# Optimization experiments

Measured on AMD Instinct MI355X. Metric: run time of the kernel, lower is better.

## Reference

```python
import jax, jax.numpy as jnp
import numpy as np

NUM_ENTS = 20000
NUM_RELS = 500
DIM = 256
BATCH = 32
GAMMA = 12.0
EPSILON = 2.0
EMB_RANGE = (GAMMA + EPSILON) / DIM  # embedding_range
PI = 3.1415926235897933


def setup_inputs() -> dict:
    key = jax.random.key(0)
    k1, k2, k3, k4 = jax.random.split(key, 4)
    # xavier_normal for 2-D params: std = sqrt(2/(fan_in+fan_out))
    std_e = float(np.sqrt(2.0 / (NUM_ENTS + 2 * DIM)))
    std_r = float(np.sqrt(2.0 / (NUM_RELS + 3 * DIM)))
    emb_e = jax.random.normal(k1, (NUM_ENTS, 2 * DIM), dtype=jnp.float32) * std_e
    emb_rel = jax.random.normal(k2, (NUM_RELS, 3 * DIM), dtype=jnp.float32) * std_r
    e1 = jax.random.randint(k3, (BATCH,), 0, NUM_ENTS, dtype=jnp.int32)
    rel = jax.random.randint(k4, (BATCH,), 0, NUM_RELS, dtype=jnp.int32)
    e2_multi = jax.random.uniform(jax.random.fold_in(key, 7), (BATCH, NUM_ENTS), dtype=jnp.float32)
    phase_weight = jnp.full((1, 1), 0.5 * EMB_RANGE, dtype=jnp.float32)
    modulus_weight = jnp.full((1, 1), 1.0, dtype=jnp.float32)
    return {
        "g": 0,
        "e1": e1,
        "rel": rel,
        "e2_multi": e2_multi,
        "emb_e": emb_e,
        "emb_rel": emb_rel,
        "phase_weight": phase_weight,
        "modulus_weight": modulus_weight,
    }


def reference(g, e1, rel, e2_multi, emb_e, emb_rel, phase_weight, modulus_weight):
    head = emb_e[e1]            # (B, 2D)
    r = emb_rel[rel]            # (B, 3D)
    tail = emb_e                # (N, 2D)

    phase_head, mod_head = jnp.split(head, 2, axis=-1)            # (B, D) each
    phase_rel, mod_rel, bias_rel = jnp.split(r, 3, axis=-1)       # (B, D) each
    phase_tail, mod_tail = jnp.split(tail, 2, axis=-1)            # (N, D) each

    scale = EMB_RANGE / PI
    phase_head = phase_head / scale
    phase_rel = phase_rel / scale
    phase_tail = phase_tail / scale

    # (B, N, D) broadcast
    phase_score = (phase_head + phase_rel)[:, None, :] - phase_tail[None, :, :]

    mod_rel = jnp.abs(mod_rel)
    bias_rel = jnp.minimum(bias_rel, 1.0)
    bias_rel = jnp.where(bias_rel < -mod_rel, -mod_rel, bias_rel)

    r_score = (mod_head * (mod_rel + bias_rel))[:, None, :] \
        - mod_tail[None, :, :] * (1.0 - bias_rel)[:, None, :]      # (B, N, D)

    phase_term = jnp.sum(jnp.abs(jnp.sin(phase_score / 2.0)), axis=-1) * phase_weight  # (B, N)
    r_term = jnp.linalg.norm(r_score, axis=-1) * modulus_weight                          # (B, N)

    return jax.nn.sigmoid(GAMMA - (phase_term + r_term))
```

## Files before the change

### kernel.cpp

```cpp
#include <hip/hip_runtime.h>
#include <math.h>


#define D_   256
#define N_   20000
#define NT   16
#define NBLK (N_ / NT)
#define AP   264

#define K2S 4.571428571428571f

typedef short short8 __attribute__((ext_vector_type(8)));
typedef float f32x4  __attribute__((ext_vector_type(4)));

__device__ __forceinline__ float sinrev_(float x) { return __builtin_amdgcn_sinf(x); }

__device__ __forceinline__ short bf16r(float x) {
    union { float f; unsigned u; } v; v.f = x;
    unsigned r = (v.u + 0x7FFFu + ((v.u >> 16) & 1u)) >> 16;
    return (short)r;
}

__device__ __forceinline__ short8 pack8(float4 a, float4 b, bool sq) {
    float v[8] = {a.x, a.y, a.z, a.w, b.x, b.y, b.z, b.w};
    short8 r;
#pragma unroll
    for (int i = 0; i < 8; ++i) { float x = sq ? v[i] * v[i] : v[i]; r[i] = bf16r(x); }
    return r;
}

__global__ __launch_bounds__(512, 6)
void hake_fused(const int* __restrict__ e1, const int* __restrict__ rel,
                const float* __restrict__ emb_e, const float* __restrict__ emb_rel,
                const float* __restrict__ pw_p, const float* __restrict__ mw_p,
                float* __restrict__ out)
{
    __shared__ short A1[32 * AP];
    __shared__ short A2[32 * AP];
    __shared__ float U[4352];
    __shared__ float S0p[16][32];
    __shared__ float S0[32];

    const int t  = threadIdx.x;
    const int l  = t & 63;
    const int w  = t >> 6;
    const int b  = t & 31;
    const int g  = t >> 5;
    const int d0 = g * 16;
    const int fr = l & 15;
    const int hi = l >> 4;
    const int n0 = blockIdx.x * NT;

    const int term  = w >> 2;
    const int dbase = (w & 3) * 64;
    const float* mtp = emb_e + (size_t)(n0 + fr) * (2 * D_) + D_;
    float4 bva0 = *(const float4*)(mtp + dbase + hi * 8);
    float4 bvb0 = *(const float4*)(mtp + dbase + hi * 8 + 4);
    float4 bva1 = *(const float4*)(mtp + dbase + 32 + hi * 8);
    float4 bvb1 = *(const float4*)(mtp + dbase + 32 + hi * 8 + 4);

    const float* prow0 = emb_e + (size_t)(n0 + w * 2) * (2 * D_);
    const float* prow1 = emb_e + (size_t)(n0 + w * 2 + 1) * (2 * D_);
    float4 pv0 = *(const float4*)(prow0 + l * 4);
    float4 pv1 = *(const float4*)(prow1 + l * 4);

    float ar[16];
    {
        const int he = e1[b], hr = rel[b];
        const float* be = emb_e  + (size_t)he * (2 * D_);
        const float* br = emb_rel + (size_t)hr * (3 * D_);
        float a1v[16], a2v[16];
        float s0 = 0.0f;
#pragma unroll
        for (int q = 0; q < 4; ++q) {
            float4 ph4 = *(const float4*)(be + d0 + q * 4);
            float4 pq4 = *(const float4*)(br + d0 + q * 4);
            float4 mh4 = *(const float4*)(be + D_ + d0 + q * 4);
            float4 mr4 = *(const float4*)(br + D_ + d0 + q * 4);
            float4 bi4 = *(const float4*)(br + 2 * D_ + d0 + q * 4);
            float phv[4] = {ph4.x, ph4.y, ph4.z, ph4.w};
            float pqv[4] = {pq4.x, pq4.y, pq4.z, pq4.w};
            float mhv[4] = {mh4.x, mh4.y, mh4.z, mh4.w};
            float mrv[4] = {mr4.x, mr4.y, mr4.z, mr4.w};
            float biv[4] = {bi4.x, bi4.y, bi4.z, bi4.w};
#pragma unroll
            for (int k = 0; k < 4; ++k) {
                const int i = q * 4 + k;
                ar[i] = (phv[k] + pqv[k]) * K2S;
                float mr = fabsf(mrv[k]);
                float bi = fminf(biv[k], 1.0f);
                bi = (bi < -mr) ? -mr : bi;
                float cc = 1.0f - bi;
                float mh = mhv[k] * (mr + bi);
                a1v[i] = cc * cc;
                a2v[i] = -2.0f * mh * cc;
                s0 = fmaf(mh, mh, s0);
            }
        }
        short8 w1a, w1b, w2a, w2b;
#pragma unroll
        for (int i = 0; i < 8; ++i) {
            w1a[i] = bf16r(a1v[i]);     w1b[i] = bf16r(a1v[8 + i]);
            w2a[i] = bf16r(a2v[i]);     w2b[i] = bf16r(a2v[8 + i]);
        }
        *(short8*)(&A1[b * AP + d0])     = w1a;
        *(short8*)(&A1[b * AP + d0 + 8]) = w1b;
        *(short8*)(&A2[b * AP + d0])     = w2a;
        *(short8*)(&A2[b * AP + d0 + 8]) = w2b;
        S0p[g][b] = s0;
    }
    __syncthreads();

    if (t < 32) {
        float s = 0.0f;
#pragma unroll
        for (int q = 0; q < 16; ++q) s += S0p[q][t];
        S0[t] = s;
    }

    {
        short8 bf0 = pack8(bva0, bvb0, term == 0);
        short8 bf1 = pack8(bva1, bvb1, term == 0);
        const short* At = term ? A2 : A1;
        short8 a00 = *(const short8*)(At + fr * AP + dbase + hi * 8);
        short8 a01 = *(const short8*)(At + fr * AP + dbase + 32 + hi * 8);
        short8 a10 = *(const short8*)(At + (16 + fr) * AP + dbase + hi * 8);
        short8 a11 = *(const short8*)(At + (16 + fr) * AP + dbase + 32 + hi * 8);
        f32x4 acc0 = {0.f, 0.f, 0.f, 0.f};
        f32x4 acc1 = {0.f, 0.f, 0.f, 0.f};
        acc0 = __builtin_amdgcn_mfma_f32_16x16x32_bf16(a00, bf0, acc0, 0, 0, 0);
        acc0 = __builtin_amdgcn_mfma_f32_16x16x32_bf16(a01, bf1, acc0, 0, 0, 0);
        acc1 = __builtin_amdgcn_mfma_f32_16x16x32_bf16(a10, bf0, acc1, 0, 0, 0);
        acc1 = __builtin_amdgcn_mfma_f32_16x16x32_bf16(a11, bf1, acc1, 0, 0, 0);
#pragma unroll
        for (int r = 0; r < 4; ++r) {
            U[(w * 32 + hi * 4 + r) * 17 + fr]      = acc0[r];
            U[(w * 32 + 16 + hi * 4 + r) * 17 + fr] = acc1[r];
        }
    }
    __syncthreads();

    const int fn = t >> 5, fb = t & 31;
    float rr = 0.0f;
#pragma unroll
    for (int ww = 0; ww < 8; ++ww) rr += U[(ww * 32 + fb) * 17 + fn];
    __syncthreads();

    float4* Pp = (float4*)U;
    Pp[(w * 2) * 64 + l]     = make_float4(pv0.x * K2S, pv0.y * K2S, pv0.z * K2S, pv0.w * K2S);
    Pp[(w * 2 + 1) * 64 + l] = make_float4(pv1.x * K2S, pv1.y * K2S, pv1.z * K2S, pv1.w * K2S);
    __syncthreads();

    float sph[NT];
#pragma unroll
    for (int j = 0; j < NT; ++j) sph[j] = 0.0f;
#pragma unroll
    for (int q = 0; q < 4; ++q) {
#pragma unroll
        for (int j = 0; j < NT; ++j) {
            float4 tv = Pp[j * 64 + g * 4 + q];
            sph[j] += fabsf(sinrev_(ar[q * 4 + 0] - tv.x));
            sph[j] += fabsf(sinrev_(ar[q * 4 + 1] - tv.y));
            sph[j] += fabsf(sinrev_(ar[q * 4 + 2] - tv.z));
            sph[j] += fabsf(sinrev_(ar[q * 4 + 3] - tv.w));
        }
    }

#pragma unroll
    for (int j = 0; j < NT; ++j) sph[j] += __shfl_xor(sph[j], 32, 64);
    __syncthreads();
    if (l < 32) {
#pragma unroll
        for (int j = 0; j < NT; ++j) U[(w * 16 + j) * 32 + l] = sph[j];
    }
    __syncthreads();

    {
        float pa = 0.0f;
#pragma unroll
        for (int ww = 0; ww < 8; ++ww) pa += U[(ww * 16 + fn) * 32 + fb];
        float rfull = fmaxf(rr + S0[fb], 0.0f);
        float z = fmaf(pa, pw_p[0], sqrtf(rfull) * mw_p[0]) - 12.0f;
        out[(size_t)fb * N_ + (n0 + fn)] = 1.0f / (1.0f + __expf(z));
    }
}

extern "C" void kernel_launch(void* const* d_in, const int* in_sizes, int n_in,
                              void* d_out, int out_size, void* d_ws, size_t ws_size,
                              hipStream_t stream)
{
    const int*   e1      = (const int*)d_in[1];
    const int*   rel     = (const int*)d_in[2];
    const float* emb_e   = (const float*)d_in[4];
    const float* emb_rel = (const float*)d_in[5];
    const float* pw      = (const float*)d_in[6];
    const float* mw      = (const float*)d_in[7];
    float* out = (float*)d_out;

    hipLaunchKernelGGL(hake_fused, dim3(NBLK), dim3(512), 0, stream,
                       e1, rel, emb_e, emb_rel, pw, mw, out);
}
```

Before: 41.76 us.

## Replace per-pair sine with angle-difference identity using precomputed sin/cos

```diff
diff --git a/kernel.cpp b/kernel.cpp
--- a/kernel.cpp
+++ b/kernel.cpp
@@ -14,6 +14,7 @@
 typedef float f32x4  __attribute__((ext_vector_type(4)));
 
 __device__ __forceinline__ float sinrev_(float x) { return __builtin_amdgcn_sinf(x); }
+__device__ __forceinline__ float cosrev_(float x) { return __builtin_amdgcn_cosf(x); }
 
 __device__ __forceinline__ short bf16r(float x) {
     union { float f; unsigned u; } v; v.f = x;
@@ -35,11 +36,13 @@
                 const float* __restrict__ pw_p, const float* __restrict__ mw_p,
                 float* __restrict__ out)
 {
-    __shared__ short A1[32 * AP];
-    __shared__ short A2[32 * AP];
+    __shared__ __align__(16) char ABP[2 * 32 * AP * 2];
     __shared__ float U[4352];
     __shared__ float S0p[16][32];
     __shared__ float S0[32];
+
+    short* A1 = (short*)ABP;
+    short* A2 = (short*)(ABP + 32 * AP * 2);
 
     const int t  = threadIdx.x;
     const int l  = t & 63;
@@ -61,32 +64,29 @@
 
     const float* prow0 = emb_e + (size_t)(n0 + w * 2) * (2 * D_);
     const float* prow1 = emb_e + (size_t)(n0 + w * 2 + 1) * (2 * D_);
-    float4 pv0 = *(const float4*)(prow0 + l * 4);
-    float4 pv1 = *(const float4*)(prow1 + l * 4);
-
-    float ar[16];
-    {
-        const int he = e1[b], hr = rel[b];
-        const float* be = emb_e  + (size_t)he * (2 * D_);
-        const float* br = emb_rel + (size_t)hr * (3 * D_);
+    float2 lp00 = *(const float2*)(prow0 + 2 * l);
+    float2 lp01 = *(const float2*)(prow0 + 128 + 2 * l);
+    float2 lp10 = *(const float2*)(prow1 + 2 * l);
+    float2 lp11 = *(const float2*)(prow1 + 128 + 2 * l);
+
+    const int he = e1[b], hr = rel[b];
+    const float* be = emb_e  + (size_t)he * (2 * D_);
+    const float* br = emb_rel + (size_t)hr * (3 * D_);
+
+    {
         float a1v[16], a2v[16];
         float s0 = 0.0f;
 #pragma unroll
         for (int q = 0; q < 4; ++q) {
-            float4 ph4 = *(const float4*)(be + d0 + q * 4);
-            float4 pq4 = *(const float4*)(br + d0 + q * 4);
             float4 mh4 = *(const float4*)(be + D_ + d0 + q * 4);
             float4 mr4 = *(const float4*)(br + D_ + d0 + q * 4);
             float4 bi4 = *(const float4*)(br + 2 * D_ + d0 + q * 4);
-            float phv[4] = {ph4.x, ph4.y, ph4.z, ph4.w};
-            float pqv[4] = {pq4.x, pq4.y, pq4.z, pq4.w};
             float mhv[4] = {mh4.x, mh4.y, mh4.z, mh4.w};
             float mrv[4] = {mr4.x, mr4.y, mr4.z, mr4.w};
             float biv[4] = {bi4.x, bi4.y, bi4.z, bi4.w};
 #pragma unroll
             for (int k = 0; k < 4; ++k) {
                 const int i = q * 4 + k;
-                ar[i] = (phv[k] + pqv[k]) * K2S;
                 float mr = fabsf(mrv[k]);
                 float bi = fminf(biv[k], 1.0f);
                 bi = (bi < -mr) ? -mr : bi;
@@ -146,29 +146,54 @@
     for (int ww = 0; ww < 8; ++ww) rr += U[(ww * 32 + fb) * 17 + fn];
     __syncthreads();
 
-    float4* Pp = (float4*)U;
-    Pp[(w * 2) * 64 + l]     = make_float4(pv0.x * K2S, pv0.y * K2S, pv0.z * K2S, pv0.w * K2S);
-    Pp[(w * 2 + 1) * 64 + l] = make_float4(pv1.x * K2S, pv1.y * K2S, pv1.z * K2S, pv1.w * K2S);
+    float sa[16], ca[16];
+#pragma unroll
+    for (int q = 0; q < 4; ++q) {
+        float4 ph4 = *(const float4*)(be + d0 + q * 4);
+        float4 pq4 = *(const float4*)(br + d0 + q * 4);
+        float av[4] = {(ph4.x + pq4.x) * K2S, (ph4.y + pq4.y) * K2S,
+                       (ph4.z + pq4.z) * K2S, (ph4.w + pq4.w) * K2S};
+#pragma unroll
+        for (int k = 0; k < 4; ++k) {
+            sa[q * 4 + k] = sinrev_(av[k]);
+            ca[q * 4 + k] = cosrev_(av[k]);
+        }
+    }
+
+    float4* Pf = (float4*)ABP;
+    {
+        float2 lps[4] = {lp00, lp01, lp10, lp11};
+#pragma unroll
+        for (int r2 = 0; r2 < 2; ++r2) {
+#pragma unroll
+            for (int h = 0; h < 2; ++h) {
+                float2 lp = lps[r2 * 2 + h];
+                float b0 = lp.x * K2S, b1 = lp.y * K2S;
+                Pf[(w * 2 + r2) * 128 + h * 64 + l] =
+                    make_float4(sinrev_(b0), cosrev_(b0), sinrev_(b1), cosrev_(b1));
+            }
+        }
+    }
     __syncthreads();
 
     float sph[NT];
 #pragma unroll
     for (int j = 0; j < NT; ++j) sph[j] = 0.0f;
-#pragma unroll
-    for (int q = 0; q < 4; ++q) {
+
+#pragma unroll
+    for (int dd = 0; dd < 8; ++dd) {
 #pragma unroll
         for (int j = 0; j < NT; ++j) {
-            float4 tv = Pp[j * 64 + g * 4 + q];
-            sph[j] += fabsf(sinrev_(ar[q * 4 + 0] - tv.x));
-            sph[j] += fabsf(sinrev_(ar[q * 4 + 1] - tv.y));
-            sph[j] += fabsf(sinrev_(ar[q * 4 + 2] - tv.z));
-            sph[j] += fabsf(sinrev_(ar[q * 4 + 3] - tv.w));
+            float4 tv = Pf[j * 128 + g * 8 + dd];
+            float s0 = fmaf(-ca[2 * dd],     tv.x, sa[2 * dd]     * tv.y);
+            float s1 = fmaf(-ca[2 * dd + 1], tv.z, sa[2 * dd + 1] * tv.w);
+            sph[j] += fabsf(s0);
+            sph[j] += fabsf(s1);
         }
     }
 
 #pragma unroll
     for (int j = 0; j < NT; ++j) sph[j] += __shfl_xor(sph[j], 32, 64);
-    __syncthreads();
     if (l < 32) {
 #pragma unroll
         for (int j = 0; j < NT; ++j) U[(w * 16 + j) * 32 + l] = sph[j];
```

Measured after the change: 40.74 us. 2.4% less time.

## Split head prep into separate kernel and use sin-difference identity for phase term

Applied to the files above, without the earlier changes.

```diff
diff --git a/kernel.cpp b/kernel.cpp
--- a/kernel.cpp
+++ b/kernel.cpp
@@ -6,40 +6,77 @@
 #define N_   20000
 #define NT   16
 #define NBLK (N_ / NT)
-#define AP   264
 
 #define K2S 4.571428571428571f
+
+#define WS_A1 0
+#define WS_A2 16384
+#define WS_SC 32768
+#define WS_S0 65536
 
 typedef short short8 __attribute__((ext_vector_type(8)));
 typedef float f32x4  __attribute__((ext_vector_type(4)));
 
 __device__ __forceinline__ float sinrev_(float x) { return __builtin_amdgcn_sinf(x); }
-
-__device__ __forceinline__ short bf16r(float x) {
+__device__ __forceinline__ float cosrev_(float x) { return __builtin_amdgcn_cosf(x); }
+__device__ __forceinline__ float asf_(unsigned u) { union { unsigned u; float f; } v; v.u = u; return v.f; }
+
+__device__ __forceinline__ unsigned short bf16r(float x) {
     union { float f; unsigned u; } v; v.f = x;
-    unsigned r = (v.u + 0x7FFFu + ((v.u >> 16) & 1u)) >> 16;
-    return (short)r;
+    return (unsigned short)((v.u + 0x7FFFu + ((v.u >> 16) & 1u)) >> 16);
 }
 
 __device__ __forceinline__ short8 pack8(float4 a, float4 b, bool sq) {
     float v[8] = {a.x, a.y, a.z, a.w, b.x, b.y, b.z, b.w};
     short8 r;
 #pragma unroll
-    for (int i = 0; i < 8; ++i) { float x = sq ? v[i] * v[i] : v[i]; r[i] = bf16r(x); }
+    for (int i = 0; i < 8; ++i) { float x = sq ? v[i] * v[i] : v[i]; r[i] = (short)bf16r(x); }
     return r;
 }
 
-__global__ __launch_bounds__(512, 6)
-void hake_fused(const int* __restrict__ e1, const int* __restrict__ rel,
-                const float* __restrict__ emb_e, const float* __restrict__ emb_rel,
-                const float* __restrict__ pw_p, const float* __restrict__ mw_p,
-                float* __restrict__ out)
+__global__ __launch_bounds__(256)
+void hake_prep(const int* __restrict__ e1, const int* __restrict__ rel,
+               const float* __restrict__ emb_e, const float* __restrict__ emb_rel,
+               char* __restrict__ ws)
 {
-    __shared__ short A1[32 * AP];
-    __shared__ short A2[32 * AP];
+    __shared__ float sp[4];
+    const int b = blockIdx.x, d = threadIdx.x;
+    const int he = e1[b], hr = rel[b];
+    const float ph = emb_e[(size_t)he * 512 + d];
+    const float mh = emb_e[(size_t)he * 512 + 256 + d];
+    const float pr = emb_rel[(size_t)hr * 768 + d];
+    const float mr = emb_rel[(size_t)hr * 768 + 256 + d];
+    const float bi = emb_rel[(size_t)hr * 768 + 512 + d];
+
+    const float a = (ph + pr) * K2S;
+    ((unsigned*)(ws + WS_SC))[b * 256 + d] =
+        ((unsigned)bf16r(cosrev_(a)) << 16) | (unsigned)bf16r(sinrev_(a));
+
+    const float mra = fabsf(mr);
+    float bic = fminf(bi, 1.0f);
+    bic = (bic < -mra) ? -mra : bic;
+    const float cc  = 1.0f - bic;
+    const float mhp = mh * (mra + bic);
+    ((short*)(ws + WS_A1))[b * 256 + d] = (short)bf16r(cc * cc);
+    ((short*)(ws + WS_A2))[b * 256 + d] = (short)bf16r(-2.0f * mhp * cc);
+
+    float s0 = mhp * mhp;
+#pragma unroll
+    for (int o = 1; o < 64; o <<= 1) s0 += __shfl_xor(s0, o, 64);
+    if ((threadIdx.x & 63) == 0) sp[threadIdx.x >> 6] = s0;
+    __syncthreads();
+    if (threadIdx.x == 0)
+        ((float*)(ws + WS_S0))[b] = sp[0] + sp[1] + sp[2] + sp[3];
+}
+
+__global__ __launch_bounds__(512, 8)
+void hake_main(const float* __restrict__ emb_e,
+               const char* __restrict__ ws,
+               const float* __restrict__ pw_p, const float* __restrict__ mw_p,
+               float* __restrict__ out)
+{
+    __shared__ unsigned Pb[NT * 256];
     __shared__ float U[4352];
-    __shared__ float S0p[16][32];
-    __shared__ float S0[32];
 
     const int t  = threadIdx.x;
     const int l  = t & 63;
@@ -51,6 +88,11 @@
     const int hi = l >> 4;
     const int n0 = blockIdx.x * NT;
 
+    const short*    A1w = (const short*)(ws + WS_A1);
+    const short*    A2w = (const short*)(ws + WS_A2);
+    const unsigned* SCw = (const unsigned*)(ws + WS_SC);
+    const float*    S0w = (const float*)(ws + WS_S0);
+
     const int term  = w >> 2;
     const int dbase = (w & 3) * 64;
     const float* mtp = emb_e + (size_t)(n0 + fr) * (2 * D_) + D_;
@@ -61,71 +103,44 @@
 
     const float* prow0 = emb_e + (size_t)(n0 + w * 2) * (2 * D_);
     const float* prow1 = emb_e + (size_t)(n0 + w * 2 + 1) * (2 * D_);
-    float4 pv0 = *(const float4*)(prow0 + l * 4);
-    float4 pv1 = *(const float4*)(prow1 + l * 4);
-
-    float ar[16];
-    {
-        const int he = e1[b], hr = rel[b];
-        const float* be = emb_e  + (size_t)he * (2 * D_);
-        const float* br = emb_rel + (size_t)hr * (3 * D_);
-        float a1v[16], a2v[16];
-        float s0 = 0.0f;
-#pragma unroll
-        for (int q = 0; q < 4; ++q) {
-            float4 ph4 = *(const float4*)(be + d0 + q * 4);
-            float4 pq4 = *(const float4*)(br + d0 + q * 4);
-            float4 mh4 = *(const float4*)(be + D_ + d0 + q * 4);
-            float4 mr4 = *(const float4*)(br + D_ + d0 + q * 4);
-            float4 bi4 = *(const float4*)(br + 2 * D_ + d0 + q * 4);
-            float phv[4] = {ph4.x, ph4.y, ph4.z, ph4.w};
-            float pqv[4] = {pq4.x, pq4.y, pq4.z, pq4.w};
-            float mhv[4] = {mh4.x, mh4.y, mh4.z, mh4.w};
-            float mrv[4] = {mr4.x, mr4.y, mr4.z, mr4.w};
-            float biv[4] = {bi4.x, bi4.y, bi4.z, bi4.w};
-#pragma unroll
-            for (int k = 0; k < 4; ++k) {
-                const int i = q * 4 + k;
-                ar[i] = (phv[k] + pqv[k]) * K2S;
-                float mr = fabsf(mrv[k]);
-                float bi = fminf(biv[k], 1.0f);
-                bi = (bi < -mr) ? -mr : bi;
-                float cc = 1.0f - bi;
-                float mh = mhv[k] * (mr + bi);
-                a1v[i] = cc * cc;
-                a2v[i] = -2.0f * mh * cc;
-                s0 = fmaf(mh, mh, s0);
-            }
-        }
-        short8 w1a, w1b, w2a, w2b;
-#pragma unroll
-        for (int i = 0; i < 8; ++i) {
-            w1a[i] = bf16r(a1v[i]);     w1b[i] = bf16r(a1v[8 + i]);
-            w2a[i] = bf16r(a2v[i]);     w2b[i] = bf16r(a2v[8 + i]);
-        }
-        *(short8*)(&A1[b * AP + d0])     = w1a;
-        *(short8*)(&A1[b * AP + d0 + 8]) = w1b;
-        *(short8*)(&A2[b * AP + d0])     = w2a;
-        *(short8*)(&A2[b * AP + d0 + 8]) = w2b;
-        S0p[g][b] = s0;
-    }
-    __syncthreads();
-
-    if (t < 32) {
-        float s = 0.0f;
-#pragma unroll
-        for (int q = 0; q < 16; ++q) s += S0p[q][t];
-        S0[t] = s;
+    float2 lp00 = *(const float2*)(prow0 + 2 * l);
+    float2 lp01 = *(const float2*)(prow0 + 128 + 2 * l);
+    float2 lp10 = *(const float2*)(prow1 + 2 * l);
+    float2 lp11 = *(const float2*)(prow1 + 128 + 2 * l);
+
+    const short* At = term ? A2w : A1w;
+    short8 a00 = *(const short8*)(At + fr * 256 + dbase + hi * 8);
+    short8 a01 = *(const short8*)(At + fr * 256 + dbase + 32 + hi * 8);
+    short8 a10 = *(const short8*)(At + (16 + fr) * 256 + dbase + hi * 8);
+    short8 a11 = *(const short8*)(At + (16 + fr) * 256 + dbase + 32 + hi * 8);
+
+    {
+        float s, c; unsigned u0, u1;
+        s = sinrev_(lp00.x * K2S); c = cosrev_(lp00.x * K2S);
+        u0 = ((unsigned)bf16r(c) << 16) | (unsigned)bf16r(s);
+        s = sinrev_(lp00.y * K2S); c = cosrev_(lp00.y * K2S);
+        u1 = ((unsigned)bf16r(c) << 16) | (unsigned)bf16r(s);
+        *(uint2*)(&Pb[(w * 2) * 256 + 2 * l]) = make_uint2(u0, u1);
+        s = sinrev_(lp01.x * K2S); c = cosrev_(lp01.x * K2S);
+        u0 = ((unsigned)bf16r(c) << 16) | (unsigned)bf16r(s);
+        s = sinrev_(lp01.y * K2S); c = cosrev_(lp01.y * K2S);
+        u1 = ((unsigned)bf16r(c) << 16) | (unsigned)bf16r(s);
+        *(uint2*)(&Pb[(w * 2) * 256 + 128 + 2 * l]) = make_uint2(u0, u1);
+        s = sinrev_(lp10.x * K2S); c = cosrev_(lp10.x * K2S);
+        u0 = ((unsigned)bf16r(c) << 16) | (unsigned)bf16r(s);
+        s = sinrev_(lp10.y * K2S); c = cosrev_(lp10.y * K2S);
+        u1 = ((unsigned)bf16r(c) << 16) | (unsigned)bf16r(s);
+        *(uint2*)(&Pb[(w * 2 + 1) * 256 + 2 * l]) = make_uint2(u0, u1);
+        s = sinrev_(lp11.x * K2S); c = cosrev_(lp11.x * K2S);
+        u0 = ((unsigned)bf16r(c) << 16) | (unsigned)bf16r(s);
+        s = sinrev_(lp11.y * K2S); c = cosrev_(lp11.y * K2S);
+        u1 = ((unsigned)bf16r(c) << 16) | (unsigned)bf16r(s);
+        *(uint2*)(&Pb[(w * 2 + 1) * 256 + 128 + 2 * l]) = make_uint2(u0, u1);
     }
 
     {
         short8 bf0 = pack8(bva0, bvb0, term == 0);
         short8 bf1 = pack8(bva1, bvb1, term == 0);
-        const short* At = term ? A2 : A1;
-        short8 a00 = *(const short8*)(At + fr * AP + dbase + hi * 8);
-        short8 a01 = *(const short8*)(At + fr * AP + dbase + 32 + hi * 8);
-        short8 a10 = *(const short8*)(At + (16 + fr) * AP + dbase + hi * 8);
-        short8 a11 = *(const short8*)(At + (16 + fr) * AP + dbase + 32 + hi * 8);
         f32x4 acc0 = {0.f, 0.f, 0.f, 0.f};
         f32x4 acc1 = {0.f, 0.f, 0.f, 0.f};
         acc0 = __builtin_amdgcn_mfma_f32_16x16x32_bf16(a00, bf0, acc0, 0, 0, 0);
@@ -144,25 +159,41 @@
     float rr = 0.0f;
 #pragma unroll
     for (int ww = 0; ww < 8; ++ww) rr += U[(ww * 32 + fb) * 17 + fn];
-    __syncthreads();
-
-    float4* Pp = (float4*)U;
-    Pp[(w * 2) * 64 + l]     = make_float4(pv0.x * K2S, pv0.y * K2S, pv0.z * K2S, pv0.w * K2S);
-    Pp[(w * 2 + 1) * 64 + l] = make_float4(pv1.x * K2S, pv1.y * K2S, pv1.z * K2S, pv1.w * K2S);
-    __syncthreads();
+
+    unsigned scp[16];
+    {
+        uint4 s0 = *(const uint4*)(SCw + b * 256 + d0);
+        uint4 s1 = *(const uint4*)(SCw + b * 256 + d0 + 4);
+        uint4 s2 = *(const uint4*)(SCw + b * 256 + d0 + 8);
+        uint4 s3 = *(const uint4*)(SCw + b * 256 + d0 + 12);
+        scp[0] = s0.x; scp[1] = s0.y; scp[2]  = s0.z; scp[3]  = s0.w;
+        scp[4] = s1.x; scp[5] = s1.y; scp[6]  = s1.z; scp[7]  = s1.w;
+        scp[8] = s2.x; scp[9] = s2.y; scp[10] = s2.z; scp[11] = s2.w;
+        scp[12] = s3.x; scp[13] = s3.y; scp[14] = s3.z; scp[15] = s3.w;
+    }
 
     float sph[NT];
 #pragma unroll
     for (int j = 0; j < NT; ++j) sph[j] = 0.0f;
+
 #pragma unroll
     for (int q = 0; q < 4; ++q) {
+        float saq0 = asf_(scp[q * 4 + 0] << 16), caq0 = asf_(scp[q * 4 + 0] & 0xFFFF0000u);
+        float saq1 = asf_(scp[q * 4 + 1] << 16), caq1 = asf_(scp[q * 4 + 1] & 0xFFFF0000u);
+        float saq2 = asf_(scp[q * 4 + 2] << 16), caq2 = asf_(scp[q * 4 + 2] & 0xFFFF0000u);
+        float saq3 = asf_(scp[q * 4 + 3] << 16), caq3 = asf_(scp[q * 4 + 3] & 0xFFFF0000u);
 #pragma unroll
         for (int j = 0; j < NT; ++j) {
-            float4 tv = Pp[j * 64 + g * 4 + q];
-            sph[j] += fabsf(sinrev_(ar[q * 4 + 0] - tv.x));
-            sph[j] += fabsf(sinrev_(ar[q * 4 + 1] - tv.y));
-            sph[j] += fabsf(sinrev_(ar[q * 4 + 2] - tv.z));
-            sph[j] += fabsf(sinrev_(ar[q * 4 + 3] - tv.w));
+            uint4 tv = *(const uint4*)(&Pb[j * 256 + d0 + q * 4]);
+            float sb, cb, sv;
+            sb = asf_(tv.x << 16); cb = asf_(tv.x & 0xFFFF0000u);
+            sv = fmaf(saq0, cb, -(caq0 * sb)); sph[j] += fabsf(sv);
+            sb = asf_(tv.y << 16); cb = asf_(tv.y & 0xFFFF0000u);
+            sv = fmaf(saq1, cb, -(caq1 * sb)); sph[j] += fabsf(sv);
+            sb = asf_(tv.z << 16); cb = asf_(tv.z & 0xFFFF0000u);
+            sv = fmaf(saq2, cb, -(caq2 * sb)); sph[j] += fabsf(sv);
+            sb = asf_(tv.w << 16); cb = asf_(tv.w & 0xFFFF0000u);
+            sv = fmaf(saq3, cb, -(caq3 * sb)); sph[j] += fabsf(sv);
         }
     }
 
@@ -179,7 +210,7 @@
         float pa = 0.0f;
 #pragma unroll
         for (int ww = 0; ww < 8; ++ww) pa += U[(ww * 16 + fn) * 32 + fb];
-        float rfull = fmaxf(rr + S0[fb], 0.0f);
+        float rfull = fmaxf(rr + S0w[fb], 0.0f);
         float z = fmaf(pa, pw_p[0], sqrtf(rfull) * mw_p[0]) - 12.0f;
         out[(size_t)fb * N_ + (n0 + fn)] = 1.0f / (1.0f + __expf(z));
     }
@@ -197,6 +228,8 @@
     const float* mw      = (const float*)d_in[7];
     float* out = (float*)d_out;
 
-    hipLaunchKernelGGL(hake_fused, dim3(NBLK), dim3(512), 0, stream,
-                       e1, rel, emb_e, emb_rel, pw, mw, out);
-}
+    hipLaunchKernelGGL(hake_prep, dim3(32), dim3(256), 0, stream,
+                       e1, rel, emb_e, emb_rel, (char*)d_ws);
+    hipLaunchKernelGGL(hake_main, dim3(NBLK), dim3(512), 0, stream,
+                       emb_e, (const char*)d_ws, pw, mw, out);
+}
```

Measured after the change: 34.38 us. 1.21x faster.
